# Kernel tuning notes

Measured on AMD Instinct MI355X. Metric: run time of the kernel, lower is better.

## Reference

```python
import jax, jax.numpy as jnp
import numpy as np

B, S, D, E = 4, 2048, 1024, 8
HD = D // E          # per-expert head dim = 128
ROPE = HD // 2       # rotary dims = 64 (32 complex pairs)


def setup_inputs() -> dict:
    key = jax.random.key(0)
    ks = jax.random.split(key, 5)
    x = jax.random.normal(ks[0], (B, S, D), dtype=jnp.float32)
    Wg = jax.random.normal(ks[1], (D, E), dtype=jnp.float32) * 0.02
    Wqkv = jax.random.normal(ks[2], (E, D, 3 * HD), dtype=jnp.float32) * 0.02
    Wff = jax.random.normal(ks[3], (E, HD, D), dtype=jnp.float32) * 0.02
    b_ff = jnp.zeros((D,), dtype=jnp.float32)
    # precompute_freqs_cis(qk_rope_head_dim=ROPE, seqlen=S), theta=10000
    inv = 1.0 / (10000.0 ** (np.arange(0, ROPE, 2, dtype=np.float32) / ROPE))  # [ROPE//2]
    ang = np.arange(S, dtype=np.float32)[:, None] * inv[None, :]               # [S, ROPE//2]
    cos = jnp.asarray(np.cos(ang), dtype=jnp.float32)
    sin = jnp.asarray(np.sin(ang), dtype=jnp.float32)
    return {"x": x, "Wg": Wg, "Wqkv": Wqkv, "Wff": Wff, "b_ff": b_ff, "cos": cos, "sin": sin}


def _apply_rope(x, cos, sin):
    # x: [B,S,E,HD]; rotate the second half (x_pe), keep first half (x_nope), cat (pe, nope)
    b, s, e, hd = x.shape
    x_nope, x_pe = x[..., : hd // 2], x[..., hd // 2 :]
    xr = x_pe.reshape(b, s, e, hd // 4, 2)
    re, im = xr[..., 0], xr[..., 1]
    c = cos[None, :, None, :]
    sn = sin[None, :, None, :]
    rot = jnp.stack([re * c - im * sn, re * sn + im * c], axis=-1).reshape(b, s, e, hd // 2)
    return jnp.concatenate([rot, x_nope], axis=-1)


def reference(x, Wg, Wqkv, Wff, b_ff, cos, sin):
    b, s, d = x.shape
    e, hd = Wqkv.shape[0], Wqkv.shape[2] // 3
    # RoPE on per-expert chunks
    xh = _apply_rope(x.reshape(b, s, e, hd), cos, sin).reshape(b, s, d)
    # SwitchGate: top-1 routing
    probs = jax.nn.softmax(xh @ Wg, axis=-1)            # [b,s,E]
    expert = jnp.argmax(probs, axis=-1)                 # [b,s]
    gate = jnp.max(probs, axis=-1)                      # [b,s]
    # preprocess: per-expert stable gather of routed tokens (capacity = s, padded+masked)
    is_e = expert[None, :, :] == jnp.arange(e)[:, None, None]        # [E,b,s] bool
    order = jnp.argsort(jnp.where(is_e, 0, 1), axis=-1, stable=True)  # [E,b,s] routed-first
    mask_g = jnp.take_along_axis(is_e, order, axis=-1).astype(xh.dtype)  # [E,b,s]
    x_g = jnp.take_along_axis(xh[None], order[..., None], axis=2)    # [E,b,s,d]
    gate_g = jnp.take_along_axis(gate[None], order, axis=2)          # [E,b,s]
    # expert-grouped column-parallel QKV
    qkv = jnp.einsum("ebsd,edf->ebsf", x_g, Wqkv)                    # [E,b,s,3*hd]
    q, k, v = jnp.split(qkv, 3, axis=-1)                             # [E,b,s,hd]
    # grouped sparse attention within each expert's token set
    dot = jnp.einsum("ebqh,ebkh->ebqk", q, k) / jnp.sqrt(jnp.asarray(hd, xh.dtype))
    dot = dot - 1e6 * (1.0 - mask_g[:, :, None, :])
    attn = jax.nn.softmax(dot, axis=-1)
    ctx = jnp.einsum("ebqk,ebkh->ebqh", attn, v)                     # [E,b,s,hd]
    # row-parallel output projection, gate-weighted
    out = jnp.einsum("ebsh,ehd->ebsd", ctx, Wff) + b_ff
    out = out * (gate_g * mask_g)[..., None]
    # scatter_add combine back to [b,s,d]
    outs = jnp.zeros((b, s, d), dtype=xh.dtype)
    outs = outs.at[jnp.arange(b)[None, :, None], order].add(out)
    return outs
```

## Files before the change

### kernel.cpp

```cpp
#include <hip/hip_runtime.h>
#include <math.h>

#define Bn 4
#define Sn 2048
#define Dn 1024
#define En 8
#define HDn 128
#define NG 32
#define MAXT 160
#define MAXN 1024

typedef __attribute__((ext_vector_type(8))) short bf16x8;
typedef __attribute__((ext_vector_type(4))) float f32x4;
typedef unsigned short u16;

__device__ __forceinline__ unsigned bf16_rn(float x) {
  unsigned u = __float_as_uint(x);
  return (u + 0x7fffu + ((u >> 16) & 1u)) >> 16;
}
__device__ __forceinline__ void bsplit(float x, unsigned& hi, unsigned& lo) {
  hi = bf16_rn(x);
  lo = bf16_rn(x - __uint_as_float(hi << 16));
}
__device__ __forceinline__ void gl16(const void* g, void* l) {
  __builtin_amdgcn_global_load_lds(
      (const __attribute__((address_space(1))) void*)g,
      (__attribute__((address_space(3))) void*)l, 16, 0, 0);
}
#define MFMA16(a, b, c) __builtin_amdgcn_mfma_f32_16x16x32_bf16((a), (b), (c), 0, 0, 0)

__global__ __launch_bounds__(256) void k_rope_gate(
    const float* __restrict__ x, const float* __restrict__ Wg,
    const float* __restrict__ cosT, const float* __restrict__ sinT,
    u16* __restrict__ xh_hi, u16* __restrict__ xh_lo,
    int* __restrict__ expertArr, float* __restrict__ gateArr)
{
  int bs = blockIdx.x;
  int s  = bs & (Sn - 1);
  const float* xrow = x + (size_t)bs * Dn;
  int t = threadIdx.x;
  int j = t << 2;
  int hbase = j & ~127;
  int jj = j & 127;
  float v0, v1, v2, v3;
  if (jj < 64) {
    const float* pe = xrow + hbase + 64 + jj;
    float a0 = pe[0], a1 = pe[1], a2 = pe[2], a3 = pe[3];
    int p0 = jj >> 1;
    float c0 = cosT[s * 32 + p0],     s0 = sinT[s * 32 + p0];
    float c1 = cosT[s * 32 + p0 + 1], s1 = sinT[s * 32 + p0 + 1];
    v0 = a0 * c0 - a1 * s0;
    v1 = a0 * s0 + a1 * c0;
    v2 = a2 * c1 - a3 * s1;
    v3 = a2 * s1 + a3 * c1;
  } else {
    const float* np = xrow + hbase + (jj - 64);
    v0 = np[0]; v1 = np[1]; v2 = np[2]; v3 = np[3];
  }
  unsigned h0,l0,h1,l1,h2,l2,h3,l3;
  bsplit(v0,h0,l0); bsplit(v1,h1,l1); bsplit(v2,h2,l2); bsplit(v3,h3,l3);
  *(ushort4*)(xh_hi + (size_t)bs * Dn + j) = make_ushort4((u16)h0,(u16)h1,(u16)h2,(u16)h3);
  *(ushort4*)(xh_lo + (size_t)bs * Dn + j) = make_ushort4((u16)l0,(u16)l1,(u16)l2,(u16)l3);

  float pl[En];
  const float* wr = Wg + (size_t)j * En;
#pragma unroll
  for (int e = 0; e < En; ++e)
    pl[e] = v0 * wr[e] + v1 * wr[En + e] + v2 * wr[2 * En + e] + v3 * wr[3 * En + e];
#pragma unroll
  for (int off = 1; off < 64; off <<= 1) {
#pragma unroll
    for (int e = 0; e < En; ++e) pl[e] += __shfl_xor(pl[e], off, 64);
  }
  __shared__ float red[4][En];
  int wv = t >> 6, ln = t & 63;
  if (ln == 0) {
#pragma unroll
    for (int e = 0; e < En; ++e) red[wv][e] = pl[e];
  }
  __syncthreads();
  if (t == 0) {
    float l[En];
    for (int e = 0; e < En; ++e) l[e] = red[0][e] + red[1][e] + red[2][e] + red[3][e];
    float m = l[0]; int be = 0;
    for (int e = 1; e < En; ++e) if (l[e] > m) { m = l[e]; be = e; }
    float ss = 0.f;
    for (int e = 0; e < En; ++e) ss += expf(l[e] - m);
    expertArr[bs] = be;
    gateArr[bs] = 1.0f / ss;
  }
}

__global__ __launch_bounds__(256) void k_prep_w(
    const float* __restrict__ W, u16* __restrict__ hiT, u16* __restrict__ loT,
    int Kdim, int Ndim)
{
  int e = blockIdx.z, k0 = blockIdx.x << 6, c0 = blockIdx.y << 6;
  __shared__ float tile[64][65];
  int t = threadIdx.x;
  int r = t >> 4, cc = (t & 15) << 2;
  const float* src = W + ((size_t)e * Kdim + k0) * Ndim + c0;
#pragma unroll
  for (int i = 0; i < 4; ++i) {
    float4 v = *(const float4*)(src + (size_t)(r + i * 16) * Ndim + cc);
    tile[r + i * 16][cc + 0] = v.x; tile[r + i * 16][cc + 1] = v.y;
    tile[r + i * 16][cc + 2] = v.z; tile[r + i * 16][cc + 3] = v.w;
  }
  __syncthreads();
#pragma unroll
  for (int i = 0; i < 4; ++i) {
    int oc = (t >> 4) + i * 16;
    int ok = (t & 15) << 2;
    float v0 = tile[ok + 0][oc], v1 = tile[ok + 1][oc];
    float v2 = tile[ok + 2][oc], v3 = tile[ok + 3][oc];
    unsigned h0,l0,h1,l1,h2,l2,h3,l3;
    bsplit(v0,h0,l0); bsplit(v1,h1,l1); bsplit(v2,h2,l2); bsplit(v3,h3,l3);
    size_t o = ((size_t)e * Ndim + c0 + oc) * Kdim + k0 + ok;
    *(ushort4*)(hiT + o) = make_ushort4((u16)h0,(u16)h1,(u16)h2,(u16)h3);
    *(ushort4*)(loT + o) = make_ushort4((u16)l0,(u16)l1,(u16)l2,(u16)l3);
  }
}

__global__ __launch_bounds__(256) void k_route(
    const int* __restrict__ expertArr, int* __restrict__ idx, int* __restrict__ cnt)
{
  int g = blockIdx.x;
  int b = g >> 3, e = g & 7;
  int t = threadIdx.x;
  __shared__ int wtot[4];
  __shared__ int base;
  if (t == 0) base = 0;
  __syncthreads();
  for (int c = 0; c < Sn; c += 256) {
    int s = c + t;
    int pred = (expertArr[b * Sn + s] == e) ? 1 : 0;
    unsigned long long mask = __ballot(pred);
    int ln = t & 63, wv = t >> 6;
    int wpre = __popcll(mask & ((1ull << ln) - 1ull));
    if (ln == 63) wtot[wv] = wpre + pred;
    __syncthreads();
    int woff = 0;
    for (int w = 0; w < wv; ++w) woff += wtot[w];
    int tot = wtot[0] + wtot[1] + wtot[2] + wtot[3];
    if (pred) idx[(g << 11) + base + woff + wpre] = s;
    __syncthreads();
    if (t == 0) base += tot;
    __syncthreads();
  }
  if (t == 0) cnt[g] = base;
}

__global__ void k_tiles(const int* __restrict__ cnt, int* __restrict__ tileg,
                        int* __restrict__ tilem, int* __restrict__ ntile)
{
  if (threadIdx.x == 0 && blockIdx.x == 0) {
    int t = 0;
    for (int g = 0; g < NG; ++g) {
      int n = cnt[g];
      for (int m0 = 0; m0 < n && t < MAXT; m0 += 64) { tileg[t] = g; tilem[t] = m0; ++t; }
    }
    ntile[0] = t;
  }
}

__global__ __launch_bounds__(256) void k_qkv(
    const u16* __restrict__ xh_hi, const u16* __restrict__ xh_lo,
    const u16* __restrict__ WqT_hi, const u16* __restrict__ WqT_lo,
    const int* __restrict__ idx, const int* __restrict__ cnt,
    const int* __restrict__ tileg, const int* __restrict__ tilem,
    const int* __restrict__ ntile,
    u16* __restrict__ qkv_hi, u16* __restrict__ qkv_lo,
    u16* __restrict__ vT_hi, u16* __restrict__ vT_lo)
{
  extern __shared__ unsigned char LDS[];
  int tid = blockIdx.x;
  if (tid >= ntile[0]) return;
  int g = tileg[tid], m0 = tilem[tid];
  int n = cnt[g];
  int b = g >> 3, e = g & 7;
  const int* idxg = idx + (g << 11);
  int n0 = blockIdx.y << 6;
  int t = threadIdx.x;
  int wid = t >> 6, l = t & 63;
  int wr = wid >> 1, wc = wid & 1;
  int lc = l & 15, lq = l >> 4;

  int q0 = wid * 2, q1 = q0 + 1;
  int rl0 = q0 * 8 + (l >> 3), rl1 = q1 * 8 + (l >> 3);
  int kt0 = ((l & 7) ^ (rl0 & 7)) * 8;
  int kt1 = ((l & 7) ^ (rl1 & 7)) * 8;
  int rg0 = m0 + rl0; rg0 = rg0 < n ? rg0 : n - 1;
  int rg1 = m0 + rl1; rg1 = rg1 < n ? rg1 : n - 1;
  size_t aoff0 = ((size_t)(b * Sn + idxg[rg0])) * Dn + kt0;
  size_t aoff1 = ((size_t)(b * Sn + idxg[rg1])) * Dn + kt1;
  size_t boff0 = ((size_t)e * 384 + n0 + rl0) * Dn + kt0;
  size_t boff1 = ((size_t)e * 384 + n0 + rl1) * Dn + kt1;
  int dq0 = q0 << 10, dq1 = q1 << 10;

  f32x4 acc[2][2];
#pragma unroll
  for (int i = 0; i < 2; ++i)
#pragma unroll
    for (int j = 0; j < 2; ++j) acc[i][j] = (f32x4){0.f, 0.f, 0.f, 0.f};

  int rA0 = wr * 32 + lc, rA1 = rA0 + 16;
  int cB0 = wc * 32 + lc, cB1 = cB0 + 16;
  int sw = lc & 7;

#define STAGE(bufb, k0)                                                      \
  do {                                                                       \
    unsigned bb = (bufb);                                                    \
    gl16(xh_hi + aoff0 + (k0), LDS + bb + dq0);                              \
    gl16(xh_hi + aoff1 + (k0), LDS + bb + dq1);                              \
    gl16(xh_lo + aoff0 + (k0), LDS + bb + 8192 + dq0);                       \
    gl16(xh_lo + aoff1 + (k0), LDS + bb + 8192 + dq1);                       \
    gl16(WqT_hi + boff0 + (k0), LDS + bb + 16384 + dq0);                     \
    gl16(WqT_hi + boff1 + (k0), LDS + bb + 16384 + dq1);                     \
    gl16(WqT_lo + boff0 + (k0), LDS + bb + 24576 + dq0);                     \
    gl16(WqT_lo + boff1 + (k0), LDS + bb + 24576 + dq1);                     \
  } while (0)

  STAGE(0, 0);
  __syncthreads();
  for (int tt = 0; tt < 16; ++tt) {
    unsigned cur = (tt & 1) ? 32768u : 0u;
    if (tt < 15) STAGE(cur ^ 32768u, (tt + 1) * 64);
#pragma unroll
    for (int ks = 0; ks < 2; ++ks) {
      int sl = ks * 4 + lq;
      int sx = (sl ^ sw) << 4;
      int a0b = cur + rA0 * 128 + sx;
      int a1b = cur + rA1 * 128 + sx;
      int b0b = cur + 16384 + cB0 * 128 + sx;
      int b1b = cur + 16384 + cB1 * 128 + sx;
      bf16x8 ah0 = *(const bf16x8*)(LDS + a0b);
      bf16x8 ah1 = *(const bf16x8*)(LDS + a1b);
      bf16x8 al0 = *(const bf16x8*)(LDS + a0b + 8192);
      bf16x8 al1 = *(const bf16x8*)(LDS + a1b + 8192);
      bf16x8 bh0 = *(const bf16x8*)(LDS + b0b);
      bf16x8 bh1 = *(const bf16x8*)(LDS + b1b);
      bf16x8 bl0 = *(const bf16x8*)(LDS + b0b + 8192);
      bf16x8 bl1 = *(const bf16x8*)(LDS + b1b + 8192);
      acc[0][0] = MFMA16(ah0, bh0, acc[0][0]);
      acc[0][1] = MFMA16(ah0, bh1, acc[0][1]);
      acc[1][0] = MFMA16(ah1, bh0, acc[1][0]);
      acc[1][1] = MFMA16(ah1, bh1, acc[1][1]);
      acc[0][0] = MFMA16(al0, bh0, acc[0][0]);
      acc[0][1] = MFMA16(al0, bh1, acc[0][1]);
      acc[1][0] = MFMA16(al1, bh0, acc[1][0]);
      acc[1][1] = MFMA16(al1, bh1, acc[1][1]);
      acc[0][0] = MFMA16(ah0, bl0, acc[0][0]);
      acc[0][1] = MFMA16(ah0, bl1, acc[0][1]);
      acc[1][0] = MFMA16(ah1, bl0, acc[1][0]);
      acc[1][1] = MFMA16(ah1, bl1, acc[1][1]);
    }
    __syncthreads();
  }
#undef STAGE

#pragma unroll
  for (int fi = 0; fi < 2; ++fi) {
#pragma unroll
    for (int rr = 0; rr < 4; ++rr) {
      int rg = m0 + wr * 32 + fi * 16 + lq * 4 + rr;
      if (rg < n) {
        int tok = idxg[rg];
#pragma unroll
        for (int fj = 0; fj < 2; ++fj) {
          int col = n0 + wc * 32 + fj * 16 + lc;
          unsigned h, lo2;
          bsplit(acc[fi][fj][rr], h, lo2);
          if (col < 256) {
            size_t o = (size_t)(b * Sn + tok) * 384 + col;
            qkv_hi[o] = (u16)h; qkv_lo[o] = (u16)lo2;
          } else {
            size_t o = ((size_t)g * HDn + (col - 256)) * MAXN + rg;
            vT_hi[o] = (u16)h; vT_lo[o] = (u16)lo2;
          }
        }
      }
    }
  }
}

__global__ __launch_bounds__(256) void k_attn(
    const u16* __restrict__ qkv_hi, const u16* __restrict__ qkv_lo,
    const u16* __restrict__ vT_hi, const u16* __restrict__ vT_lo,
    const int* __restrict__ idx, const int* __restrict__ cnt,
    const int* __restrict__ tileg, const int* __restrict__ tilem,
    const int* __restrict__ ntile,
    u16* __restrict__ ctx_hi, u16* __restrict__ ctx_lo)
{
  extern __shared__ unsigned char LDS[];
  int tid = blockIdx.x;
  if (tid >= ntile[0]) return;
  int g = tileg[tid], m0 = tilem[tid];
  int n = cnt[g];
  int b = g >> 3;
  const int* idxg = idx + (g << 11);
  int t = threadIdx.x, wid = t >> 6, l = t & 63;
  int lc = l & 15, lq = l >> 4;
  const float scale = 0.08838834764831845f;

  int qrg = m0 + wid * 16 + lc; qrg = qrg < n ? qrg : n - 1;
  size_t qoff = (size_t)(b * Sn + idxg[qrg]) * 384 + lq * 8;
  bf16x8 Qhi[4], Qlo[4];
#pragma unroll
  for (int ks = 0; ks < 4; ++ks) {
    Qhi[ks] = *(const bf16x8*)(qkv_hi + qoff + ks * 32);
    Qlo[ks] = *(const bf16x8*)(qkv_lo + qoff + ks * 32);
  }

  f32x4 acc[8];
#pragma unroll
  for (int i = 0; i < 8; ++i) acc[i] = (f32x4){0.f, 0.f, 0.f, 0.f};
  float m_r[4] = {-1e30f, -1e30f, -1e30f, -1e30f};
  float l_r[4] = {0.f, 0.f, 0.f, 0.f};

  size_t vbase = ((size_t)g * HDn + lc) * MAXN + lq * 8;
  unsigned pbase = 65536u + wid * 4096u;

#define STAGEK(bufb, kc)                                                     \
  do {                                                                       \
    unsigned bb = (bufb);                                                    \
    for (int j = 0; j < 4; ++j) {                                            \
      int c = wid * 4 + j;                                                   \
      int row = (kc) + c * 4 + lq;                                           \
      int rg = row < n ? row : n - 1;                                        \
      int srcslot = lc ^ (((c & 1) << 2) | lq);                              \
      size_t soff = (size_t)(b * Sn + idxg[rg]) * 384 + 128 + srcslot * 8;   \
      gl16(qkv_hi + soff, LDS + bb + c * 1024);                              \
      gl16(qkv_lo + soff, LDS + bb + 16384 + c * 1024);                      \
    }                                                                        \
  } while (0)

  int nt = (n + 63) >> 6;
  STAGEK(0, 0);
  __syncthreads();

  for (int tt = 0; tt < nt; ++tt) {
    unsigned cur = (tt & 1) ? 32768u : 0u;
    if (tt + 1 < nt) STAGEK(cur ^ 32768u, (tt + 1) * 64);
    int kc = tt * 64;

    f32x4 Sf[4];
#pragma unroll
    for (int kf = 0; kf < 4; ++kf) Sf[kf] = (f32x4){0.f, 0.f, 0.f, 0.f};
#pragma unroll
    for (int ks = 0; ks < 4; ++ks) {
#pragma unroll
      for (int kf = 0; kf < 4; ++kf) {
        int row = kf * 16 + lc;
        unsigned byte = cur + row * 256 + ((((ks << 2) | lq) ^ (row & 7)) << 4);
        bf16x8 kh = *(const bf16x8*)(LDS + byte);
        bf16x8 kl = *(const bf16x8*)(LDS + byte + 16384);
        Sf[kf] = MFMA16(Qhi[ks], kh, Sf[kf]);
        Sf[kf] = MFMA16(Qlo[ks], kh, Sf[kf]);
        Sf[kf] = MFMA16(Qhi[ks], kl, Sf[kf]);
      }
    }

    float mloc[4] = {-1e30f, -1e30f, -1e30f, -1e30f};
#pragma unroll
    for (int kf = 0; kf < 4; ++kf) {
#pragma unroll
      for (int r = 0; r < 4; ++r) {
        int key = kc + kf * 16 + lc;
        float s = (key < n) ? Sf[kf][r] * scale : -1e30f;
        Sf[kf][r] = s;
        mloc[r] = fmaxf(mloc[r], s);
      }
    }
#pragma unroll
    for (int off = 1; off < 16; off <<= 1) {
#pragma unroll
      for (int r = 0; r < 4; ++r) mloc[r] = fmaxf(mloc[r], __shfl_xor(mloc[r], off, 64));
    }
    float corr[4], rs[4] = {0.f, 0.f, 0.f, 0.f};
#pragma unroll
    for (int r = 0; r < 4; ++r) {
      float mn = fmaxf(m_r[r], mloc[r]);
      corr[r] = expf(m_r[r] - mn);
      m_r[r] = mn;
    }
#pragma unroll
    for (int kf = 0; kf < 4; ++kf) {
#pragma unroll
      for (int r = 0; r < 4; ++r) {
        float p = expf(Sf[kf][r] - m_r[r]);
        rs[r] += p;
        unsigned ph, plo;
        bsplit(p, ph, plo);
        int prow = (lq << 2) | r;
        int slot = (kf << 1) | (lc >> 3);
        unsigned pb = pbase + prow * 128 + ((slot ^ (prow & 7)) << 4) + ((lc & 7) << 1);
        *(u16*)(LDS + pb) = (u16)ph;
        *(u16*)(LDS + pb + 2048) = (u16)plo;
      }
    }
#pragma unroll
    for (int off = 1; off < 16; off <<= 1) {
#pragma unroll
      for (int r = 0; r < 4; ++r) rs[r] += __shfl_xor(rs[r], off, 64);
    }
#pragma unroll
    for (int r = 0; r < 4; ++r) l_r[r] = l_r[r] * corr[r] + rs[r];
#pragma unroll
    for (int df = 0; df < 8; ++df)
#pragma unroll
      for (int r = 0; r < 4; ++r) acc[df][r] *= corr[r];

#pragma unroll
    for (int ks2 = 0; ks2 < 2; ++ks2) {
      unsigned pr = pbase + lc * 128 + ((((ks2 << 2) | lq) ^ (lc & 7)) << 4);
      bf16x8 pa = *(const bf16x8*)(LDS + pr);
      bf16x8 pl = *(const bf16x8*)(LDS + pr + 2048);
#pragma unroll
      for (int df = 0; df < 8; ++df) {
        size_t vo = vbase + (size_t)(df * 16) * MAXN + kc + ks2 * 32;
        bf16x8 vh = *(const bf16x8*)(vT_hi + vo);
        bf16x8 vl = *(const bf16x8*)(vT_lo + vo);
        acc[df] = MFMA16(pa, vh, acc[df]);
        acc[df] = MFMA16(pl, vh, acc[df]);
        acc[df] = MFMA16(pa, vl, acc[df]);
      }
    }
    __syncthreads();
  }
#undef STAGEK

#pragma unroll
  for (int r = 0; r < 4; ++r) {
    int rg = m0 + wid * 16 + (lq << 2) + r;
    if (rg < n) {
      int tok = idxg[rg];
      float inv = 1.0f / l_r[r];
      size_t o = (size_t)(b * Sn + tok) * HDn + lc;
#pragma unroll
      for (int df = 0; df < 8; ++df) {
        unsigned h, lo2;
        bsplit(acc[df][r] * inv, h, lo2);
        ctx_hi[o + df * 16] = (u16)h;
        ctx_lo[o + df * 16] = (u16)lo2;
      }
    }
  }
}

__global__ __launch_bounds__(256) void k_out(
    const u16* __restrict__ ctx_hi, const u16* __restrict__ ctx_lo,
    const u16* __restrict__ WfT_hi, const u16* __restrict__ WfT_lo,
    const float* __restrict__ bff,
    const int* __restrict__ idx, const int* __restrict__ cnt,
    const int* __restrict__ tileg, const int* __restrict__ tilem,
    const int* __restrict__ ntile,
    const float* __restrict__ gateArr,
    float* __restrict__ out)
{
  int tid = blockIdx.x;
  if (tid >= ntile[0]) return;
  int g = tileg[tid], m0 = tilem[tid];
  int n = cnt[g];
  int b = g >> 3, e = g & 7;
  const int* idxg = idx + (g << 11);
  int t = threadIdx.x, wid = t >> 6, l = t & 63;
  int lc = l & 15, lq = l >> 4;
  int n0 = blockIdx.y * 256 + wid * 64;

  f32x4 acc[4][4];
#pragma unroll
  for (int i = 0; i < 4; ++i)
#pragma unroll
    for (int j = 0; j < 4; ++j) acc[i][j] = (f32x4){0.f, 0.f, 0.f, 0.f};

  size_t aoff[4];
#pragma unroll
  for (int fi = 0; fi < 4; ++fi) {
    int rg = m0 + fi * 16 + lc; rg = rg < n ? rg : n - 1;
    aoff[fi] = ((size_t)(b * Sn + idxg[rg])) * HDn + lq * 8;
  }
  size_t boff[4];
#pragma unroll
  for (int fj = 0; fj < 4; ++fj)
    boff[fj] = ((size_t)e * Dn + n0 + fj * 16 + lc) * HDn + lq * 8;

#pragma unroll
  for (int ks = 0; ks < 4; ++ks) {
    int ko = ks * 32;
    bf16x8 ah[4], al[4], bh[4], bl[4];
#pragma unroll
    for (int fi = 0; fi < 4; ++fi) {
      ah[fi] = *(const bf16x8*)(ctx_hi + aoff[fi] + ko);
      al[fi] = *(const bf16x8*)(ctx_lo + aoff[fi] + ko);
    }
#pragma unroll
    for (int fj = 0; fj < 4; ++fj) {
      bh[fj] = *(const bf16x8*)(WfT_hi + boff[fj] + ko);
      bl[fj] = *(const bf16x8*)(WfT_lo + boff[fj] + ko);
    }
#pragma unroll
    for (int fi = 0; fi < 4; ++fi)
#pragma unroll
      for (int fj = 0; fj < 4; ++fj) {
        acc[fi][fj] = MFMA16(ah[fi], bh[fj], acc[fi][fj]);
        acc[fi][fj] = MFMA16(al[fi], bh[fj], acc[fi][fj]);
        acc[fi][fj] = MFMA16(ah[fi], bl[fj], acc[fi][fj]);
      }
  }

  float bv[4];
#pragma unroll
  for (int fj = 0; fj < 4; ++fj) bv[fj] = bff[n0 + fj * 16 + lc];

#pragma unroll
  for (int fi = 0; fi < 4; ++fi) {
#pragma unroll
    for (int rr = 0; rr < 4; ++rr) {
      int rg = m0 + fi * 16 + lq * 4 + rr;
      if (rg < n) {
        int tok = idxg[rg];
        float gt = gateArr[b * Sn + tok];
        float* orow = out + ((size_t)(b * Sn + tok)) * Dn + n0 + lc;
#pragma unroll
        for (int fj = 0; fj < 4; ++fj)
          orow[fj * 16] = (acc[fi][fj][rr] + bv[fj]) * gt;
      }
    }
  }
}

extern "C" void kernel_launch(void* const* d_in, const int* in_sizes, int n_in,
                              void* d_out, int out_size, void* d_ws, size_t ws_size,
                              hipStream_t stream) {
  const float* x    = (const float*)d_in[0];
  const float* Wg   = (const float*)d_in[1];
  const float* Wqkv = (const float*)d_in[2];
  const float* Wff  = (const float*)d_in[3];
  const float* bff  = (const float*)d_in[4];
  const float* cosT = (const float*)d_in[5];
  const float* sinT = (const float*)d_in[6];
  float* out = (float*)d_out;

  size_t off = 0;
  auto carve = [&](size_t bytes) -> void* {
    void* p = (char*)d_ws + off;
    off += (bytes + 255) & ~(size_t)255;
    return p;
  };
  u16* xh_hi  = (u16*)carve((size_t)Bn * Sn * Dn * 2);
  u16* xh_lo  = (u16*)carve((size_t)Bn * Sn * Dn * 2);
  u16* WqT_hi = (u16*)carve((size_t)En * 384 * Dn * 2);
  u16* WqT_lo = (u16*)carve((size_t)En * 384 * Dn * 2);
  u16* WfT_hi = (u16*)carve((size_t)En * Dn * HDn * 2);
  u16* WfT_lo = (u16*)carve((size_t)En * Dn * HDn * 2);
  u16* qkv_hi = (u16*)carve((size_t)Bn * Sn * 384 * 2);
  u16* qkv_lo = (u16*)carve((size_t)Bn * Sn * 384 * 2);
  u16* vT_hi  = (u16*)carve((size_t)NG * HDn * MAXN * 2);
  u16* vT_lo  = (u16*)carve((size_t)NG * HDn * MAXN * 2);
  u16* ctx_hi = (u16*)carve((size_t)Bn * Sn * HDn * 2);
  u16* ctx_lo = (u16*)carve((size_t)Bn * Sn * HDn * 2);
  float* gateArr = (float*)carve((size_t)Bn * Sn * sizeof(float));
  int*   expertA = (int*)carve((size_t)Bn * Sn * sizeof(int));
  int*   idx     = (int*)carve((size_t)NG * Sn * sizeof(int));
  int*   cnt     = (int*)carve((size_t)NG * sizeof(int));
  int*   tileg   = (int*)carve((size_t)MAXT * sizeof(int));
  int*   tilem   = (int*)carve((size_t)MAXT * sizeof(int));
  int*   ntile   = (int*)carve(256);
  (void)ws_size; (void)in_sizes; (void)n_in; (void)out_size;

  hipFuncSetAttribute((const void*)k_attn, hipFuncAttributeMaxDynamicSharedMemorySize, 81920);

  k_rope_gate<<<dim3(Bn * Sn), dim3(256), 0, stream>>>(x, Wg, cosT, sinT, xh_hi, xh_lo, expertA, gateArr);
  k_prep_w<<<dim3(16, 6, 8), dim3(256), 0, stream>>>(Wqkv, WqT_hi, WqT_lo, Dn, 384);
  k_prep_w<<<dim3(2, 16, 8), dim3(256), 0, stream>>>(Wff, WfT_hi, WfT_lo, HDn, Dn);
  k_route<<<dim3(NG), dim3(256), 0, stream>>>(expertA, idx, cnt);
  k_tiles<<<dim3(1), dim3(64), 0, stream>>>(cnt, tileg, tilem, ntile);
  k_qkv<<<dim3(MAXT, 6), dim3(256), 65536, stream>>>(xh_hi, xh_lo, WqT_hi, WqT_lo, idx, cnt, tileg, tilem, ntile, qkv_hi, qkv_lo, vT_hi, vT_lo);
  k_attn<<<dim3(MAXT), dim3(256), 81920, stream>>>(qkv_hi, qkv_lo, vT_hi, vT_lo, idx, cnt, tileg, tilem, ntile, ctx_hi, ctx_lo);
  k_out<<<dim3(MAXT, 4), dim3(256), 0, stream>>>(ctx_hi, ctx_lo, WfT_hi, WfT_lo, bff, idx, cnt, tileg, tilem, ntile, gateArr, out);
}
```

Baseline: 185.0 us.

## Use one wavefront per token in rope-gate and halve QKV GEMM K-tile

```diff
diff --git a/kernel.cpp b/kernel.cpp
--- a/kernel.cpp
+++ b/kernel.cpp
@@ -35,57 +35,71 @@
     u16* __restrict__ xh_hi, u16* __restrict__ xh_lo,
     int* __restrict__ expertArr, float* __restrict__ gateArr)
 {
-  int bs = blockIdx.x;
+  int wid = threadIdx.x >> 6, l = threadIdx.x & 63;
+  int bs = (blockIdx.x << 2) + wid;
   int s  = bs & (Sn - 1);
   const float* xrow = x + (size_t)bs * Dn;
-  int t = threadIdx.x;
-  int j = t << 2;
-  int hbase = j & ~127;
-  int jj = j & 127;
-  float v0, v1, v2, v3;
+  int j0 = l << 4;
+  int hb = j0 & ~127;
+  int jj = j0 & 127;
+  float v[16];
   if (jj < 64) {
-    const float* pe = xrow + hbase + 64 + jj;
-    float a0 = pe[0], a1 = pe[1], a2 = pe[2], a3 = pe[3];
+    const float* pe = xrow + hb + 64 + jj;
+    float a[16];
+    *(float4*)(a + 0)  = *(const float4*)(pe + 0);
+    *(float4*)(a + 4)  = *(const float4*)(pe + 4);
+    *(float4*)(a + 8)  = *(const float4*)(pe + 8);
+    *(float4*)(a + 12) = *(const float4*)(pe + 12);
     int p0 = jj >> 1;
-    float c0 = cosT[s * 32 + p0],     s0 = sinT[s * 32 + p0];
-    float c1 = cosT[s * 32 + p0 + 1], s1 = sinT[s * 32 + p0 + 1];
-    v0 = a0 * c0 - a1 * s0;
-    v1 = a0 * s0 + a1 * c0;
-    v2 = a2 * c1 - a3 * s1;
-    v3 = a2 * s1 + a3 * c1;
+#pragma unroll
+    for (int i = 0; i < 8; ++i) {
+      float c  = cosT[s * 32 + p0 + i];
+      float sn = sinT[s * 32 + p0 + i];
+      v[2 * i]     = a[2 * i] * c - a[2 * i + 1] * sn;
+      v[2 * i + 1] = a[2 * i] * sn + a[2 * i + 1] * c;
+    }
   } else {
-    const float* np = xrow + hbase + (jj - 64);
-    v0 = np[0]; v1 = np[1]; v2 = np[2]; v3 = np[3];
-  }
-  unsigned h0,l0,h1,l1,h2,l2,h3,l3;
-  bsplit(v0,h0,l0); bsplit(v1,h1,l1); bsplit(v2,h2,l2); bsplit(v3,h3,l3);
-  *(ushort4*)(xh_hi + (size_t)bs * Dn + j) = make_ushort4((u16)h0,(u16)h1,(u16)h2,(u16)h3);
-  *(ushort4*)(xh_lo + (size_t)bs * Dn + j) = make_ushort4((u16)l0,(u16)l1,(u16)l2,(u16)l3);
-
-  float pl[En];
-  const float* wr = Wg + (size_t)j * En;
-#pragma unroll
-  for (int e = 0; e < En; ++e)
-    pl[e] = v0 * wr[e] + v1 * wr[En + e] + v2 * wr[2 * En + e] + v3 * wr[3 * En + e];
+    const float* np = xrow + hb + (jj - 64);
+    *(float4*)(v + 0)  = *(const float4*)(np + 0);
+    *(float4*)(v + 4)  = *(const float4*)(np + 4);
+    *(float4*)(v + 8)  = *(const float4*)(np + 8);
+    *(float4*)(v + 12) = *(const float4*)(np + 12);
+  }
+  u16 hh[16] __attribute__((aligned(16)));
+  u16 ll[16] __attribute__((aligned(16)));
+#pragma unroll
+  for (int i = 0; i < 16; ++i) {
+    unsigned h, lo;
+    bsplit(v[i], h, lo);
+    hh[i] = (u16)h; ll[i] = (u16)lo;
+  }
+  *(uint4*)(xh_hi + (size_t)bs * Dn + j0)     = *(uint4*)(hh);
+  *(uint4*)(xh_hi + (size_t)bs * Dn + j0 + 8) = *(uint4*)(hh + 8);
+  *(uint4*)(xh_lo + (size_t)bs * Dn + j0)     = *(uint4*)(ll);
+  *(uint4*)(xh_lo + (size_t)bs * Dn + j0 + 8) = *(uint4*)(ll + 8);
+
+  float pl[8] = {0.f, 0.f, 0.f, 0.f, 0.f, 0.f, 0.f, 0.f};
+  const float* wr = Wg + (size_t)j0 * En;
+#pragma unroll
+  for (int i = 0; i < 16; ++i) {
+    float4 w0 = *(const float4*)(wr + i * 8);
+    float4 w1 = *(const float4*)(wr + i * 8 + 4);
+    float xv = v[i];
+    pl[0] += xv * w0.x; pl[1] += xv * w0.y; pl[2] += xv * w0.z; pl[3] += xv * w0.w;
+    pl[4] += xv * w1.x; pl[5] += xv * w1.y; pl[6] += xv * w1.z; pl[7] += xv * w1.w;
+  }
 #pragma unroll
   for (int off = 1; off < 64; off <<= 1) {
 #pragma unroll
-    for (int e = 0; e < En; ++e) pl[e] += __shfl_xor(pl[e], off, 64);
-  }
-  __shared__ float red[4][En];
-  int wv = t >> 6, ln = t & 63;
-  if (ln == 0) {
-#pragma unroll
-    for (int e = 0; e < En; ++e) red[wv][e] = pl[e];
-  }
-  __syncthreads();
-  if (t == 0) {
-    float l[En];
-    for (int e = 0; e < En; ++e) l[e] = red[0][e] + red[1][e] + red[2][e] + red[3][e];
-    float m = l[0]; int be = 0;
-    for (int e = 1; e < En; ++e) if (l[e] > m) { m = l[e]; be = e; }
-    float ss = 0.f;
-    for (int e = 0; e < En; ++e) ss += expf(l[e] - m);
+    for (int e = 0; e < 8; ++e) pl[e] += __shfl_xor(pl[e], off, 64);
+  }
+  float m = pl[0]; int be = 0;
+#pragma unroll
+  for (int e = 1; e < 8; ++e) if (pl[e] > m) { m = pl[e]; be = e; }
+  float ss = 0.f;
+#pragma unroll
+  for (int e = 0; e < 8; ++e) ss += expf(pl[e] - m);
+  if (l == 0) {
     expertArr[bs] = be;
     gateArr[bs] = 1.0f / ss;
   }
@@ -185,17 +199,12 @@
   int wr = wid >> 1, wc = wid & 1;
   int lc = l & 15, lq = l >> 4;
 
-  int q0 = wid * 2, q1 = q0 + 1;
-  int rl0 = q0 * 8 + (l >> 3), rl1 = q1 * 8 + (l >> 3);
-  int kt0 = ((l & 7) ^ (rl0 & 7)) * 8;
-  int kt1 = ((l & 7) ^ (rl1 & 7)) * 8;
-  int rg0 = m0 + rl0; rg0 = rg0 < n ? rg0 : n - 1;
-  int rg1 = m0 + rl1; rg1 = rg1 < n ? rg1 : n - 1;
-  size_t aoff0 = ((size_t)(b * Sn + idxg[rg0])) * Dn + kt0;
-  size_t aoff1 = ((size_t)(b * Sn + idxg[rg1])) * Dn + kt1;
-  size_t boff0 = ((size_t)e * 384 + n0 + rl0) * Dn + kt0;
-  size_t boff1 = ((size_t)e * 384 + n0 + rl1) * Dn + kt1;
-  int dq0 = q0 << 10, dq1 = q1 << 10;
+  int srow = t >> 2;
+  int sslot = (t & 3) ^ ((srow >> 1) & 3);
+  int rgs = m0 + srow; rgs = rgs < n ? rgs : n - 1;
+  size_t aoffR = ((size_t)(b * Sn + idxg[rgs])) * Dn + sslot * 8;
+  size_t boffR = ((size_t)e * 384 + n0 + srow) * Dn + sslot * 8;
+  unsigned dst = (unsigned)t << 4;
 
   f32x4 acc[2][2];
 #pragma unroll
@@ -205,55 +214,44 @@
 
   int rA0 = wr * 32 + lc, rA1 = rA0 + 16;
   int cB0 = wc * 32 + lc, cB1 = cB0 + 16;
-  int sw = lc & 7;
-
-#define STAGE(bufb, k0)                                                      \
-  do {                                                                       \
-    unsigned bb = (bufb);                                                    \
-    gl16(xh_hi + aoff0 + (k0), LDS + bb + dq0);                              \
-    gl16(xh_hi + aoff1 + (k0), LDS + bb + dq1);                              \
-    gl16(xh_lo + aoff0 + (k0), LDS + bb + 8192 + dq0);                       \
-    gl16(xh_lo + aoff1 + (k0), LDS + bb + 8192 + dq1);                       \
-    gl16(WqT_hi + boff0 + (k0), LDS + bb + 16384 + dq0);                     \
-    gl16(WqT_hi + boff1 + (k0), LDS + bb + 16384 + dq1);                     \
-    gl16(WqT_lo + boff0 + (k0), LDS + bb + 24576 + dq0);                     \
-    gl16(WqT_lo + boff1 + (k0), LDS + bb + 24576 + dq1);                     \
+  unsigned swA = (unsigned)((lq ^ ((rA0 >> 1) & 3)) << 4);
+  unsigned swB = (unsigned)((lq ^ ((cB0 >> 1) & 3)) << 4);
+  unsigned bA0 = rA0 * 64 + swA, bA1 = rA1 * 64 + swA;
+  unsigned bB0 = 8192 + cB0 * 64 + swB, bB1 = 8192 + cB1 * 64 + swB;
+
+#define STAGE(bb, k0)                                                \
+  do {                                                               \
+    gl16(xh_hi + aoffR + (k0), LDS + (bb) + dst);                    \
+    gl16(xh_lo + aoffR + (k0), LDS + (bb) + 4096 + dst);             \
+    gl16(WqT_hi + boffR + (k0), LDS + (bb) + 8192 + dst);            \
+    gl16(WqT_lo + boffR + (k0), LDS + (bb) + 12288 + dst);           \
   } while (0)
 
   STAGE(0, 0);
   __syncthreads();
-  for (int tt = 0; tt < 16; ++tt) {
-    unsigned cur = (tt & 1) ? 32768u : 0u;
-    if (tt < 15) STAGE(cur ^ 32768u, (tt + 1) * 64);
-#pragma unroll
-    for (int ks = 0; ks < 2; ++ks) {
-      int sl = ks * 4 + lq;
-      int sx = (sl ^ sw) << 4;
-      int a0b = cur + rA0 * 128 + sx;
-      int a1b = cur + rA1 * 128 + sx;
-      int b0b = cur + 16384 + cB0 * 128 + sx;
-      int b1b = cur + 16384 + cB1 * 128 + sx;
-      bf16x8 ah0 = *(const bf16x8*)(LDS + a0b);
-      bf16x8 ah1 = *(const bf16x8*)(LDS + a1b);
-      bf16x8 al0 = *(const bf16x8*)(LDS + a0b + 8192);
-      bf16x8 al1 = *(const bf16x8*)(LDS + a1b + 8192);
-      bf16x8 bh0 = *(const bf16x8*)(LDS + b0b);
-      bf16x8 bh1 = *(const bf16x8*)(LDS + b1b);
-      bf16x8 bl0 = *(const bf16x8*)(LDS + b0b + 8192);
-      bf16x8 bl1 = *(const bf16x8*)(LDS + b1b + 8192);
-      acc[0][0] = MFMA16(ah0, bh0, acc[0][0]);
-      acc[0][1] = MFMA16(ah0, bh1, acc[0][1]);
-      acc[1][0] = MFMA16(ah1, bh0, acc[1][0]);
-      acc[1][1] = MFMA16(ah1, bh1, acc[1][1]);
-      acc[0][0] = MFMA16(al0, bh0, acc[0][0]);
-      acc[0][1] = MFMA16(al0, bh1, acc[0][1]);
-      acc[1][0] = MFMA16(al1, bh0, acc[1][0]);
-      acc[1][1] = MFMA16(al1, bh1, acc[1][1]);
-      acc[0][0] = MFMA16(ah0, bl0, acc[0][0]);
-      acc[0][1] = MFMA16(ah0, bl1, acc[0][1]);
-      acc[1][0] = MFMA16(ah1, bl0, acc[1][0]);
-      acc[1][1] = MFMA16(ah1, bl1, acc[1][1]);
-    }
+  for (int tt = 0; tt < 32; ++tt) {
+    unsigned cur = (tt & 1) ? 16384u : 0u;
+    if (tt < 31) STAGE(cur ^ 16384u, (tt + 1) * 32);
+    bf16x8 ah0 = *(const bf16x8*)(LDS + cur + bA0);
+    bf16x8 ah1 = *(const bf16x8*)(LDS + cur + bA1);
+    bf16x8 al0 = *(const bf16x8*)(LDS + cur + bA0 + 4096);
+    bf16x8 al1 = *(const bf16x8*)(LDS + cur + bA1 + 4096);
+    bf16x8 bh0 = *(const bf16x8*)(LDS + cur + bB0);
+    bf16x8 bh1 = *(const bf16x8*)(LDS + cur + bB1);
+    bf16x8 bl0 = *(const bf16x8*)(LDS + cur + bB0 + 4096);
+    bf16x8 bl1 = *(const bf16x8*)(LDS + cur + bB1 + 4096);
+    acc[0][0] = MFMA16(ah0, bh0, acc[0][0]);
+    acc[0][1] = MFMA16(ah0, bh1, acc[0][1]);
+    acc[1][0] = MFMA16(ah1, bh0, acc[1][0]);
+    acc[1][1] = MFMA16(ah1, bh1, acc[1][1]);
+    acc[0][0] = MFMA16(al0, bh0, acc[0][0]);
+    acc[0][1] = MFMA16(al0, bh1, acc[0][1]);
+    acc[1][0] = MFMA16(al1, bh0, acc[1][0]);
+    acc[1][1] = MFMA16(al1, bh1, acc[1][1]);
+    acc[0][0] = MFMA16(ah0, bl0, acc[0][0]);
+    acc[0][1] = MFMA16(ah0, bl1, acc[0][1]);
+    acc[1][0] = MFMA16(ah1, bl0, acc[1][0]);
+    acc[1][1] = MFMA16(ah1, bl1, acc[1][1]);
     __syncthreads();
   }
 #undef STAGE
@@ -570,12 +568,12 @@
 
   hipFuncSetAttribute((const void*)k_attn, hipFuncAttributeMaxDynamicSharedMemorySize, 81920);
 
-  k_rope_gate<<<dim3(Bn * Sn), dim3(256), 0, stream>>>(x, Wg, cosT, sinT, xh_hi, xh_lo, expertA, gateArr);
+  k_rope_gate<<<dim3(Bn * Sn / 4), dim3(256), 0, stream>>>(x, Wg, cosT, sinT, xh_hi, xh_lo, expertA, gateArr);
   k_prep_w<<<dim3(16, 6, 8), dim3(256), 0, stream>>>(Wqkv, WqT_hi, WqT_lo, Dn, 384);
   k_prep_w<<<dim3(2, 16, 8), dim3(256), 0, stream>>>(Wff, WfT_hi, WfT_lo, HDn, Dn);
   k_route<<<dim3(NG), dim3(256), 0, stream>>>(expertA, idx, cnt);
   k_tiles<<<dim3(1), dim3(64), 0, stream>>>(cnt, tileg, tilem, ntile);
-  k_qkv<<<dim3(MAXT, 6), dim3(256), 65536, stream>>>(xh_hi, xh_lo, WqT_hi, WqT_lo, idx, cnt, tileg, tilem, ntile, qkv_hi, qkv_lo, vT_hi, vT_lo);
+  k_qkv<<<dim3(MAXT, 6), dim3(256), 32768, stream>>>(xh_hi, xh_lo, WqT_hi, WqT_lo, idx, cnt, tileg, tilem, ntile, qkv_hi, qkv_lo, vT_hi, vT_lo);
   k_attn<<<dim3(MAXT), dim3(256), 81920, stream>>>(qkv_hi, qkv_lo, vT_hi, vT_lo, idx, cnt, tileg, tilem, ntile, ctx_hi, ctx_lo);
   k_out<<<dim3(MAXT, 4), dim3(256), 0, stream>>>(ctx_hi, ctx_lo, WfT_hi, WfT_lo, bff, idx, cnt, tileg, tilem, ntile, gateArr, out);
 }
```

Result: slower. 195.3 us (+5.6%).
